# Optimization experiments

Measured on AMD Instinct MI355X. Metric: run time of the kernel, lower is better.

Reference implementation:

```python
import jax, jax.numpy as jnp
import numpy as np

N = 100000; NFEAT = 256; NHID = 128; NCLASS = 40; DEG = 16; E = N * DEG
L = 2; AH = 16; ALPHA = 0.2; LP_ALPHA = 0.5


def setup_inputs() -> dict:
    key = jax.random.key(0)
    ks = jax.random.split(key, 12)
    s = 0.05
    x = jax.random.normal(ks[0], (N, NFEAT), jnp.float32)
    row = jnp.repeat(jnp.arange(N), DEG)                       # each node has DEG out-edges
    col = jax.random.randint(ks[1], (E,), 0, N)
    edges = jnp.stack([row, col])                              # [2, E]
    degree = jax.random.uniform(ks[2], (N, 1), jnp.float32, 0.5, 1.5)
    label = jax.random.uniform(ks[3], (N, NCLASS), jnp.float32)
    return {
        "x": x, "edges": edges, "degree": degree, "iftrain": 0, "label": label,
        "lb_w": jax.random.normal(ks[4], (NHID, NFEAT)) * s,
        "lb_b": jnp.zeros((NHID,)),
        "L2F": jax.random.normal(ks[5], (NCLASS, NHID)) * s,
        "Ws": jax.random.normal(ks[6], (L, 2 * NHID, NHID)) * s,
        "w2m": jax.random.normal(ks[7], (L, AH, NHID)) * s,
        "b2m": jnp.zeros((L, AH)),
        "ab": jnp.zeros((L, 1, AH + 1)),
        "lf1w": jax.random.normal(ks[8], (L, AH, (AH + 1) * 3)) * s,
        "lf1b": jnp.zeros((L, AH)),
        "lf2w": jax.random.normal(ks[9], (L, 1, AH)) * s,
        "lf2b": jnp.zeros((L, 1)),
        "LPW": jnp.ones((L, N, 1)),
        "la2w": jax.random.normal(ks[10], (NCLASS, NHID)) * s,
        "la2b": jnp.zeros((NCLASS,)),
    }


def _seg(vals, row, n):
    return jax.ops.segment_sum(vals, row, num_segments=n)


def _layer(x, pre_label, aggr, row, col, degree, lpw, W, w2m, b2m, ab, lf1w, lf1b, lf2w, lf2b):
    n = x.shape[0]
    # final_h = aggr * spmm(adj, LP_W*h*deg) * deg + (1-aggr) * h
    h = jnp.concatenate([x, pre_label], axis=1) @ W            # [N, nhid]
    agg = _seg((lpw * h * degree)[col], row, n)
    h = aggr * agg * degree + (1.0 - aggr) * h
    rowcnt = _seg(jnp.ones((row.shape[0], 1), x.dtype), row, n)  # [N,1] edges per row

    def mini(feat):
        m = feat @ w2m.T + b2m                                 # [N, AH]
        avg = _seg(m[col], row, n) / rowcnt                    # mean neighbor feature
        dist = jnp.sqrt(jnp.sum((avg[row] - m[col]) ** 2, -1) + 1e-12)  # [E]
        d2 = (_seg(dist, row, n) / rowcnt[:, 0])[:, None]      # row-wise mean distance
        return jnp.concatenate([m, d2], axis=1)                # [N, AH+1]

    def factor(hs, hd, hdiff):
        f = jnp.tanh(jnp.concatenate([hs, hd, hdiff], 1) @ lf1w.T + lf1b)
        return jax.nn.sigmoid((f @ lf2w.T + lf2b)[:, 0])       # [E]

    m0 = mini(h)
    hs0, hd0 = m0[row], m0[col]
    hdiff = jnp.abs(hd0 - hs0)
    f0 = factor(hs0, hd0, hdiff)
    m1 = mini(x)
    f1 = factor(m1[row] + ab, m1[col] + ab, hdiff)             # note: reuses hdiff (as in torch code)
    f1hop = (_seg(f1, row, n) / rowcnt[:, 0])[:, None]         # mean-reduce spmm
    f2hop = (_seg(f0 * f1hop[col, 0], row, n) / rowcnt[:, 0])[:, None]
    return jax.nn.leaky_relu(h, ALPHA), f2hop


def reference(x, edges, degree, iftrain, label, lb_w, lb_b, L2F, Ws, w2m, b2m, ab,
              lf1w, lf1b, lf2w, lf2b, LPW, la2w, la2b):
    row, col = edges[0], edges[1]
    h = x @ lb_w.T + lb_b
    pre_label = label @ L2F
    aggr = jnp.asarray(LP_ALPHA, h.dtype)
    for l in range(L):
        h, aggr = _layer(h, pre_label, aggr, row, col, degree, LPW[l], Ws[l],
                         w2m[l], b2m[l], ab[l], lf1w[l], lf1b[l], lf2w[l], lf2b[l])
    return jax.nn.log_softmax(h @ la2w.T + la2b, axis=-1)
```

## Files before the change

kernel.cpp:

```cpp
#include <hip/hip_runtime.h>
#include <hip/hip_bf16.h>
#include <hip/hip_fp8.h>
#include <math.h>

#define NN 100000
#define NCLS 40
#define DEGC 16
#define NEDGE (NN*DEGC)
#define ALPHAC 0.2f
#define LPALPHA 0.5f

typedef short short8v __attribute__((ext_vector_type(8)));
typedef float f32x4 __attribute__((ext_vector_type(4)));

__device__ __forceinline__ short f2bf(float f) {
    unsigned u = __float_as_uint(f);
    u += 0x7fff + ((u >> 16) & 1);
    return (short)(u >> 16);
}
__device__ __forceinline__ float bf2f(ushort u) {
    return __uint_as_float(((unsigned)u) << 16);
}
__device__ __forceinline__ unsigned char f2e4m3(float f) {
    __hip_fp8_e4m3 e(f);
    return (unsigned char)e.__x;
}
__device__ __forceinline__ void e4m3x4(unsigned u, float* o) {
#pragma unroll
    for (int s = 0; s < 4; ++s) {
        __hip_fp8_e4m3 e;
        e.__x = (__hip_fp8_storage_t)((u >> (8 * s)) & 0xff);
        o[s] = (float)e;
    }
}

template <int NCH1, bool ABF, bool HASL, bool WRT8>
__global__ __launch_bounds__(256) void gemm128_lds(
    const void* __restrict__ A1v, const ushort* __restrict__ B1t,
    const ushort* __restrict__ labB64, const ushort* __restrict__ B2t,
    const float* __restrict__ bias, int leakyA, ushort* __restrict__ C,
    unsigned char* __restrict__ T8)
{
    constexpr int K1 = NCH1 * 32;
    constexpr int NG = NCH1 / 4;
    constexpr int NCH = NCH1 + (HASL ? 2 : 0);
    __shared__ __align__(16) ushort Bs1[128 * 128];
    __shared__ __align__(16) ushort Bs2[HASL ? 128 * 64 : 8];

    const int tid = threadIdx.x;
    const int l   = tid & 63;
    const int w   = tid >> 6;
    const int lr  = l & 15;
    const int lk8 = (l >> 4) << 3;
    const int n0  = blockIdx.x * 64 + w * 16;
    int r = n0 + lr; r = r < NN ? r : NN - 1;
    const int swz = (lr & 7) << 4;

    short8v afr[NCH];
    if (ABF) {
        const ushort* __restrict__ A = (const ushort*)A1v;
#pragma unroll
        for (int kc = 0; kc < NCH1; ++kc)
            afr[kc] = *(const short8v*)(A + (size_t)r * K1 + kc * 32 + lk8);
    } else {
        const float* __restrict__ A = (const float*)A1v;
#pragma unroll
        for (int g = 0; g < NCH1; g += 2) {
            const float* p0 = A + (size_t)r * K1 + g * 32 + lk8;
            const float* p1 = A + (size_t)r * K1 + (g + 1) * 32 + lk8;
            float4 a0 = *(const float4*)p0;
            float4 a1 = *(const float4*)(p0 + 4);
            float4 b0 = *(const float4*)p1;
            float4 b1 = *(const float4*)(p1 + 4);
            short8v va, vb;
            va[0] = f2bf(a0.x); va[1] = f2bf(a0.y); va[2] = f2bf(a0.z); va[3] = f2bf(a0.w);
            va[4] = f2bf(a1.x); va[5] = f2bf(a1.y); va[6] = f2bf(a1.z); va[7] = f2bf(a1.w);
            vb[0] = f2bf(b0.x); vb[1] = f2bf(b0.y); vb[2] = f2bf(b0.z); vb[3] = f2bf(b0.w);
            vb[4] = f2bf(b1.x); vb[5] = f2bf(b1.y); vb[6] = f2bf(b1.z); vb[7] = f2bf(b1.w);
            afr[g] = va;
            afr[g + 1] = vb;
        }
    }
    if (HASL) {
        afr[NCH1]     = *(const short8v*)(labB64 + (size_t)r * 64 + lk8);
        afr[NCH1 + 1] = *(const short8v*)(labB64 + (size_t)r * 64 + 32 + lk8);
    }
    if (ABF && leakyA) {
#pragma unroll
        for (int kc = 0; kc < NCH1; ++kc)
#pragma unroll
            for (int j = 0; j < 8; ++j) {
                float f = bf2f((ushort)afr[kc][j]);
                f = f > 0.f ? f : ALPHAC * f;
                afr[kc][j] = f2bf(f);
            }
    }

    if (HASL) {
#pragma unroll
        for (int s = 0; s < 4; ++s) {
            const int slot = tid + s * 256;
            const int row = slot >> 3, colq = slot & 7;
            uint4 v = *(const uint4*)(B2t + (size_t)row * 64 + colq * 8);
            *(uint4*)((char*)Bs2 + ((row * 128 + colq * 16) ^ ((row & 7) << 4))) = v;
        }
    }

    f32x4 acc[8];
#pragma unroll
    for (int ni = 0; ni < 8; ++ni) acc[ni] = (f32x4){0.f, 0.f, 0.f, 0.f};

#pragma unroll
    for (int g = 0; g < NG; ++g) {
        if (g) __syncthreads();
#pragma unroll
        for (int s = 0; s < 8; ++s) {
            const int slot = tid + s * 256;
            const int row = slot >> 4, colq = slot & 15;
            uint4 v = *(const uint4*)(B1t + (size_t)row * K1 + g * 128 + colq * 8);
            *(uint4*)((char*)Bs1 + ((row * 256 + colq * 16) ^ ((row & 7) << 4))) = v;
        }
        __syncthreads();
#pragma unroll
        for (int ni = 0; ni < 8; ++ni) {
#pragma unroll
            for (int kc = 0; kc < 4; ++kc) {
                short8v b = *(const short8v*)((const char*)Bs1 +
                    (((ni * 16 + lr) * 256 + kc * 64 + lk8 * 2) ^ swz));
                acc[ni] = __builtin_amdgcn_mfma_f32_16x16x32_bf16(afr[g * 4 + kc], b, acc[ni], 0, 0, 0);
            }
        }
    }
    if (HASL) {
#pragma unroll
        for (int ni = 0; ni < 8; ++ni) {
#pragma unroll
            for (int kc = 0; kc < 2; ++kc) {
                short8v b = *(const short8v*)((const char*)Bs2 +
                    (((ni * 16 + lr) * 128 + kc * 64 + lk8 * 2) ^ swz));
                acc[ni] = __builtin_amdgcn_mfma_f32_16x16x32_bf16(afr[NCH1 + kc], b, acc[ni], 0, 0, 0);
            }
        }
    }

    const int rsub = (l >> 4) << 2;
#pragma unroll
    for (int ni = 0; ni < 8; ++ni) {
        const int cc = ni * 16 + lr;
        const float bv = bias ? bias[cc] : 0.f;
#pragma unroll
        for (int rg = 0; rg < 4; ++rg) {
            const int rr = n0 + rsub + rg;
            if (rr < NN) {
                const float v = acc[ni][rg] + bv;
                C[(size_t)rr * 128 + cc] = (ushort)f2bf(v);
                if (WRT8) T8[(size_t)rr * 128 + cc] = f2e4m3(v);
            }
        }
    }
}

__global__ __launch_bounds__(256) void agg_v5(
    const unsigned char* __restrict__ T8, const ushort* __restrict__ hlin,
    const int* __restrict__ col, const float* __restrict__ sd,
    const float* __restrict__ degree, const float* __restrict__ aggrv,
    const float aggrs, int do_leaky, ushort* __restrict__ hout)
{
    const int lane = threadIdx.x & 63;
    const int node = blockIdx.x * 4 + (threadIdx.x >> 6);
    const int q  = lane >> 4;
    const int cq = lane & 15;

    int cl = 0; float sl = 0.f;
    if (lane < 16) {
        cl = col[node * 16 + lane];
        sl = sd[cl];
    }

    float ax[8];
#pragma unroll
    for (int s = 0; s < 8; ++s) ax[s] = 0.f;

#pragma unroll
    for (int g = 0; g < 4; ++g) {
        const int nb = g * 4 + q;
        const int   c  = __shfl(cl, nb, 64);
        const float wv = __shfl(sl, nb, 64);
        const uint2 u = *(const uint2*)(T8 + (size_t)c * 128 + cq * 8);
        float d0[4], d1[4];
        e4m3x4(u.x, d0);
        e4m3x4(u.y, d1);
#pragma unroll
        for (int s2 = 0; s2 < 4; ++s2) {
            ax[s2]     += wv * d0[s2];
            ax[4 + s2] += wv * d1[s2];
        }
    }
#pragma unroll
    for (int s = 0; s < 8; ++s) {
        ax[s] += __shfl_xor(ax[s], 16, 64);
        ax[s] += __shfl_xor(ax[s], 32, 64);
    }

    const uint4 us = *(const uint4*)(hlin + (size_t)node * 128 + cq * 8);
    const unsigned uus[4] = {us.x, us.y, us.z, us.w};
    const float a = aggrv ? aggrv[node] : aggrs;
    const float d = degree[node];
    uint4 uo;
    unsigned* uop = &uo.x;
#pragma unroll
    for (int s = 0; s < 4; ++s) {
        const int sx = (s >> 1) * 4 + (s & 1) * 2;
        float ox = a * ax[(s < 2 ? s * 2 : (s - 2) * 2 + 4)] * d;
        float oy = a * ax[(s < 2 ? s * 2 + 1 : (s - 2) * 2 + 5)] * d;
        ox += (1.f - a) * bf2f((ushort)(uus[s] & 0xffff));
        oy += (1.f - a) * bf2f((ushort)(uus[s] >> 16));
        if (do_leaky) {
            ox = ox > 0.f ? ox : ALPHAC * ox;
            oy = oy > 0.f ? oy : ALPHAC * oy;
        }
        uop[s] = (unsigned)(ushort)f2bf(ox) | ((unsigned)(ushort)f2bf(oy) << 16);
    }
    if (q == 0)
        *(uint4*)(hout + (size_t)node * 128 + cq * 8) = uo;
}

__global__ __launch_bounds__(256) void gemm16_mfma(
    const ushort* __restrict__ A, const ushort* __restrict__ Wb,
    const float* __restrict__ bias, ushort* __restrict__ Mout, int ooff)
{
    __shared__ __align__(16) ushort Wl[16 * 128];
    const int tid = threadIdx.x;
    const int l  = tid & 63;
    const int w  = tid >> 6;
    const int lr = l & 15;
    const int lk = (l >> 4) << 3;
    const int swz = (lr & 7) << 4;
    {
        const int row = tid >> 4, colq = tid & 15;
        uint4 v = *(const uint4*)(Wb + (size_t)row * 128 + colq * 8);
        *(uint4*)((char*)Wl + ((row * 256 + colq * 16) ^ ((row & 7) << 4))) = v;
    }
    const int n0 = blockIdx.x * 64 + w * 16;
    int ar = n0 + lr; ar = ar < NN ? ar : NN - 1;
    short8v a[4];
#pragma unroll
    for (int kc = 0; kc < 4; ++kc)
        a[kc] = *(const short8v*)(A + (size_t)ar * 128 + kc * 32 + lk);
    __syncthreads();
    f32x4 acc = (f32x4){0.f, 0.f, 0.f, 0.f};
#pragma unroll
    for (int kc = 0; kc < 4; ++kc) {
        short8v b = *(const short8v*)((const char*)Wl + ((lr * 256 + kc * 64 + lk * 2) ^ swz));
        acc = __builtin_amdgcn_mfma_f32_16x16x32_bf16(a[kc], b, acc, 0, 0, 0);
    }
    const float bv = bias[lr];
    const int rb = n0 + ((l >> 4) << 2);
#pragma unroll
    for (int r = 0; r < 4; ++r) {
        int rr = rb + r;
        if (rr < NN) Mout[(size_t)rr * 32 + ooff + lr] = (ushort)f2bf(acc[r] + bv);
    }
}

__global__ __launch_bounds__(256) void mini2_dual(
    const ushort* __restrict__ Mb01, const int* __restrict__ col,
    float* __restrict__ d2_0, float* __restrict__ d2_1)
{
    __shared__ float sm0[16][16][17];
    __shared__ float sm1[16][16][17];
    __shared__ float av0[16][16];
    __shared__ float av1[16][16];
    const int tid = threadIdx.x;
    const int g = tid >> 4, j = tid & 15;
    const int node = blockIdx.x * 16 + g;
    const int c = col[node * 16 + j];
    const ushort* __restrict__ rowp = Mb01 + (size_t)c * 32;
    const uint4 u0 = *(const uint4*)rowp;
    const uint4 u1 = *(const uint4*)(rowp + 8);
    const uint4 u2 = *(const uint4*)(rowp + 16);
    const uint4 u3 = *(const uint4*)(rowp + 24);
    const unsigned w0[8] = {u0.x, u0.y, u0.z, u0.w, u1.x, u1.y, u1.z, u1.w};
    const unsigned w1[8] = {u2.x, u2.y, u2.z, u2.w, u3.x, u3.y, u3.z, u3.w};
#pragma unroll
    for (int s = 0; s < 8; ++s) {
        sm0[g][j][s * 2]     = bf2f((ushort)(w0[s] & 0xffff));
        sm0[g][j][s * 2 + 1] = bf2f((ushort)(w0[s] >> 16));
        sm1[g][j][s * 2]     = bf2f((ushort)(w1[s] & 0xffff));
        sm1[g][j][s * 2 + 1] = bf2f((ushort)(w1[s] >> 16));
    }
    __syncthreads();
    float a0 = 0.f, a1 = 0.f;
#pragma unroll
    for (int nb = 0; nb < 16; ++nb) { a0 += sm0[g][nb][j]; a1 += sm1[g][nb][j]; }
    av0[g][j] = a0 * (1.f / 16.f);
    av1[g][j] = a1 * (1.f / 16.f);
    __syncthreads();
    float dd0 = 1e-12f, dd1 = 1e-12f;
#pragma unroll
    for (int d = 0; d < 16; ++d) {
        float t0 = av0[g][d] - sm0[g][j][d];
        float t1 = av1[g][d] - sm1[g][j][d];
        dd0 += t0 * t0;
        dd1 += t1 * t1;
    }
    float dist0 = sqrtf(dd0), dist1 = sqrtf(dd1);
#pragma unroll
    for (int off = 1; off < 16; off <<= 1) {
        dist0 += __shfl_xor(dist0, off, 64);
        dist1 += __shfl_xor(dist1, off, 64);
    }
    if (j == 0) {
        d2_0[node] = dist0 * (1.f / 16.f);
        d2_1[node] = dist1 * (1.f / 16.f);
    }
}

__global__ __launch_bounds__(256) void prep_pnode(
    const ushort* __restrict__ Mb01, const float* __restrict__ d2_0,
    const float* __restrict__ d2_1,
    const float* __restrict__ ab, const float* __restrict__ lf1w,
    const float* __restrict__ lf1b,
    float* __restrict__ P0s, float* __restrict__ P1s,
    unsigned char* __restrict__ PK8)
{
    const int idx = blockIdx.x * 256 + threadIdx.x;
    const int i = idx >> 4, k = idx & 15;
    float m0[17], m1a[17];
    const ushort* r0 = Mb01 + (size_t)i * 32;
    const ushort* r1 = r0 + 16;
#pragma unroll
    for (int d = 0; d < 16; ++d) {
        m0[d]  = bf2f(r0[d]);
        m1a[d] = bf2f(r1[d]) + ab[d];
    }
    m0[16]  = d2_0[i];
    m1a[16] = d2_1[i] + ab[16];
    const float* __restrict__ Wk = lf1w + k * 51;
    float p0s = lf1b[k], p1s = p0s, p0d = 0.f, p1d = 0.f;
#pragma unroll
    for (int d = 0; d < 17; ++d) {
        const float w0 = Wk[d], w1 = Wk[17 + d];
        p0s += m0[d]  * w0;  p0d += m0[d]  * w1;
        p1s += m1a[d] * w0;  p1d += m1a[d] * w1;
    }
    P0s[idx] = p0s;
    P1s[idx] = p1s;
    unsigned char* __restrict__ pk = PK8 + (size_t)i * 64;
    pk[k]      = f2e4m3(m0[k]);
    pk[16 + k] = f2e4m3(p0d);
    pk[32 + k] = f2e4m3(p1d);
    if (k == 0) *(float*)(pk + 48) = d2_0[i];
}

__global__ __launch_bounds__(256) void fact2_kernel(
    const unsigned char* __restrict__ PK8,
    const float* __restrict__ P0s, const float* __restrict__ P1s,
    const int* __restrict__ col,
    const float* __restrict__ W2c, const float* __restrict__ lf2w,
    const float* __restrict__ lf2b,
    float* __restrict__ f0out, float* __restrict__ f1hout)
{
    const int e = blockIdx.x * 256 + threadIdx.x;
    const int i = e >> 4;
    const int c = col[e];

    const unsigned char* __restrict__ pki = PK8 + (size_t)i * 64;
    const unsigned char* __restrict__ pkc = PK8 + (size_t)c * 64;
    const uint4 mi8 = *(const uint4*)pki;
    const float d2i = *(const float*)(pki + 48);
    const uint4 mc8 = *(const uint4*)pkc;
    const uint4 p08 = *(const uint4*)(pkc + 16);
    const uint4 p18 = *(const uint4*)(pkc + 32);
    const float d2c = *(const float*)(pkc + 48);

    float mi[16], mc[16], P0d[16], P1d[16];
    e4m3x4(mi8.x, mi);     e4m3x4(mi8.y, mi + 4);
    e4m3x4(mi8.z, mi + 8); e4m3x4(mi8.w, mi + 12);
    e4m3x4(mc8.x, mc);     e4m3x4(mc8.y, mc + 4);
    e4m3x4(mc8.z, mc + 8); e4m3x4(mc8.w, mc + 12);
    e4m3x4(p08.x, P0d);     e4m3x4(p08.y, P0d + 4);
    e4m3x4(p08.z, P0d + 8); e4m3x4(p08.w, P0d + 12);
    e4m3x4(p18.x, P1d);     e4m3x4(p18.y, P1d + 4);
    e4m3x4(p18.z, P1d + 8); e4m3x4(p18.w, P1d + 12);

    float2 H2[8];
#pragma unroll
    for (int k2 = 0; k2 < 8; ++k2) H2[k2] = make_float2(0.f, 0.f);
#pragma unroll
    for (int d = 0; d < 16; ++d) {
        const float hd = fabsf(mc[d] - mi[d]);
        const float2* __restrict__ wv = (const float2*)(W2c + d * 16);
#pragma unroll
        for (int k2 = 0; k2 < 8; ++k2) {
            H2[k2].x = fmaf(hd, wv[k2].x, H2[k2].x);
            H2[k2].y = fmaf(hd, wv[k2].y, H2[k2].y);
        }
    }
    {
        const float hdd = fabsf(d2c - d2i);
        const float2* __restrict__ wv = (const float2*)(W2c + 16 * 16);
#pragma unroll
        for (int k2 = 0; k2 < 8; ++k2) {
            H2[k2].x = fmaf(hdd, wv[k2].x, H2[k2].x);
            H2[k2].y = fmaf(hdd, wv[k2].y, H2[k2].y);
        }
    }
    const float* __restrict__ H = (const float*)H2;

    const float* __restrict__ p0 = P0s + (size_t)i * 16;
    const float* __restrict__ p1 = P1s + (size_t)i * 16;
    float a0 = lf2b[0], a1 = a0;
#pragma unroll
    for (int k = 0; k < 16; ++k) {
        const float t0 = p0[k] + P0d[k] + H[k];
        const float t1 = p1[k] + P1d[k] + H[k];
        const float lw = lf2w[k];
        a0 += (1.f - 2.f / (__expf(2.f * t0) + 1.f)) * lw;
        a1 += (1.f - 2.f / (__expf(2.f * t1) + 1.f)) * lw;
    }
    f0out[e] = 1.f / (1.f + __expf(-a0));
    float f1 = 1.f / (1.f + __expf(-a1));
#pragma unroll
    for (int off = 1; off < 16; off <<= 1) f1 += __shfl_xor(f1, off, 64);
    if ((threadIdx.x & 15) == 0) f1hout[i] = f1 * (1.f / 16.f);
}

__global__ void f2hop_kernel(const float* __restrict__ f0, const float* __restrict__ f1h,
                             const int* __restrict__ col, float* __restrict__ out)
{
    const int i = blockIdx.x * 256 + threadIdx.x;
    if (i >= NN) return;
    float s = 0.f;
#pragma unroll
    for (int t = 0; t < 16; ++t) {
        int e = i * 16 + t;
        s += f0[e] * f1h[col[e]];
    }
    out[i] = s * (1.f / 16.f);
}

__global__ __launch_bounds__(256) void logits_mfma(
    const ushort* __restrict__ X, const ushort* __restrict__ Wb48,
    const float* __restrict__ bias, float* __restrict__ out)
{
    __shared__ __align__(16) ushort Wl[48 * 128];
    const int tid = threadIdx.x;
    const int l  = tid & 63;
    const int w  = tid >> 6;
    const int lr = l & 15;
    const int lk = (l >> 4) << 3;
    const int swz = (lr & 7) << 4;
#pragma unroll
    for (int s = 0; s < 6; ++s) {
        const int slot = tid + s * 256;
        const int row = slot >> 4, colq = slot & 15;
        uint4 v = *(const uint4*)(Wb48 + (size_t)row * 128 + colq * 8);
        *(uint4*)((char*)Wl + ((row * 256 + colq * 16) ^ ((row & 7) << 4))) = v;
    }
    const int row_base = blockIdx.x * 128 + w * 32;
    short8v afr[2][4];
#pragma unroll
    for (int mi = 0; mi < 2; ++mi) {
        int r = row_base + mi * 16 + lr;
        r = r < NN ? r : NN - 1;
#pragma unroll
        for (int kc = 0; kc < 4; ++kc)
            afr[mi][kc] = *(const short8v*)(X + (size_t)r * 128 + kc * 32 + lk);
    }
    __syncthreads();
    f32x4 acc[2][3];
#pragma unroll
    for (int mi = 0; mi < 2; ++mi)
#pragma unroll
        for (int ni = 0; ni < 3; ++ni) acc[mi][ni] = (f32x4){0.f, 0.f, 0.f, 0.f};
#pragma unroll
    for (int ni = 0; ni < 3; ++ni) {
#pragma unroll
        for (int kc = 0; kc < 4; ++kc) {
            short8v b = *(const short8v*)((const char*)Wl +
                (((ni * 16 + lr) * 256 + kc * 64 + lk * 2) ^ swz));
#pragma unroll
            for (int mi = 0; mi < 2; ++mi)
                acc[mi][ni] = __builtin_amdgcn_mfma_f32_16x16x32_bf16(afr[mi][kc], b, acc[mi][ni], 0, 0, 0);
        }
    }

    const float b0 = bias[lr];
    const float b1 = bias[16 + lr];
    const float b2 = (lr < 8) ? bias[32 + lr] : 0.f;
    const int rsub = (l >> 4) << 2;
#pragma unroll
    for (int mi = 0; mi < 2; ++mi) {
#pragma unroll
        for (int reg = 0; reg < 4; ++reg) {
            const int row = row_base + mi * 16 + rsub + reg;
            const float z0 = acc[mi][0][reg] + b0;
            const float z1 = acc[mi][1][reg] + b1;
            const float z2 = (lr < 8) ? acc[mi][2][reg] + b2 : -1e30f;
            float m = fmaxf(fmaxf(z0, z1), z2);
#pragma unroll
            for (int off = 1; off < 16; off <<= 1) m = fmaxf(m, __shfl_xor(m, off, 64));
            float s = __expf(z0 - m) + __expf(z1 - m) + ((lr < 8) ? __expf(z2 - m) : 0.f);
#pragma unroll
            for (int off = 1; off < 16; off <<= 1) s += __shfl_xor(s, off, 64);
            const float lg = m + __logf(s);
            if (row < NN) {
                float* __restrict__ po = out + (size_t)row * NCLS;
                po[lr] = z0 - lg;
                po[16 + lr] = z1 - lg;
                if (lr < 8) po[32 + lr] = z2 - lg;
            }
        }
    }
}

__global__ void prep_misc(
    const float* __restrict__ lb_w, ushort* __restrict__ Bt0,
    const float* __restrict__ Ws, ushort* __restrict__ Wt1,
    const float* __restrict__ L2F, ushort* __restrict__ W2t,
    const float* __restrict__ la2w, ushort* __restrict__ Wb48,
    const float* __restrict__ lf1w, float* __restrict__ W2c,
    const float* __restrict__ w2m, ushort* __restrict__ W2mB,
    const float* __restrict__ LPW, const float* __restrict__ degree,
    float* __restrict__ sd2)
{
    int b = blockIdx.x;
    const int tid = threadIdx.x;
    if (b < 128) {
        int i = b * 256 + tid;
        Bt0[i] = (ushort)f2bf(lb_w[i]);
        return;
    }
    b -= 128;
    if (b < 128) {
        int i = b * 256 + tid;
        int ll = i >> 14, r = i & 16383;
        int m = r >> 7, k = r & 127;
        Wt1[i] = (ushort)f2bf(Ws[(size_t)ll * 32768 + k * 128 + m]);
        return;
    }
    b -= 128;
    if (b < 64) {
        int i = b * 256 + tid;
        int ll = i >> 13, r = i & 8191;
        int m = r >> 6, c = r & 63;
        float acc = 0.f;
        if (c < NCLS) {
            const float* Wl = Ws + (size_t)ll * 32768 + 128 * 128;
            for (int j = 0; j < 128; ++j) acc += L2F[c * 128 + j] * Wl[j * 128 + m];
        }
        W2t[i] = (ushort)f2bf(acc);
        return;
    }
    b -= 64;
    if (b < 24) {
        int i = b * 256 + tid;
        if (i < 48 * 128) {
            int c = i >> 7;
            Wb48[i] = (c < NCLS) ? (ushort)f2bf(la2w[i]) : (ushort)0;
        }
        return;
    }
    b -= 24;
    if (b < 2) {
        int t = b * 256 + tid;
        if (t < 272) {
            int d = t >> 4, k = t & 15;
            W2c[t] = lf1w[k * 51 + 34 + d];
        }
        return;
    }
    b -= 2;
    if (b < 8) {
        int i = b * 256 + tid;
        W2mB[i] = (ushort)f2bf(w2m[i]);
        return;
    }
    b -= 8;
    if (b < 391) {
        int i = b * 256 + tid;
        if (i < NN) sd2[i] = LPW[i] * degree[i];
        return;
    }
    b -= 391;
    {
        int i = b * 256 + tid;
        if (i < NN) sd2[NN + i] = LPW[NN + i] * degree[i];
    }
}

__global__ void cvt_label64v(const float* __restrict__ label, ushort* __restrict__ labB64)
{
    const int idx = blockIdx.x * 256 + threadIdx.x;
    const int i = idx >> 4;
    const int c0 = (idx & 15) * 4;
    ushort o[4];
#pragma unroll
    for (int j = 0; j < 4; ++j) {
        const int c = c0 + j;
        o[j] = (c < NCLS) ? (ushort)f2bf(label[(size_t)i * NCLS + c]) : (ushort)0;
    }
    *(uint2*)(labB64 + (size_t)i * 64 + c0) = make_uint2(
        (unsigned)o[0] | ((unsigned)o[1] << 16),
        (unsigned)o[2] | ((unsigned)o[3] << 16));
}

extern "C" void kernel_launch(void* const* d_in, const int* in_sizes, int n_in,
                              void* d_out, int out_size, void* d_ws, size_t ws_size,
                              hipStream_t stream)
{
    const float* x      = (const float*)d_in[0];
    const int*   edges  = (const int*)d_in[1];
    const float* degree = (const float*)d_in[2];
    const float* label  = (const float*)d_in[4];
    const float* lb_w   = (const float*)d_in[5];
    const float* lb_b   = (const float*)d_in[6];
    const float* L2F    = (const float*)d_in[7];
    const float* Ws     = (const float*)d_in[8];
    const float* w2m    = (const float*)d_in[9];
    const float* b2m    = (const float*)d_in[10];
    const float* ab     = (const float*)d_in[11];
    const float* lf1w   = (const float*)d_in[12];
    const float* lf1b   = (const float*)d_in[13];
    const float* lf2w   = (const float*)d_in[14];
    const float* lf2b   = (const float*)d_in[15];
    const float* LPW    = (const float*)d_in[16];
    const float* la2w   = (const float*)d_in[17];
    const float* la2b   = (const float*)d_in[18];
    const int* colp = edges + NEDGE;

    float* ws = (float*)d_ws;
    size_t o = 0;
    float* d2_0B = ws + o; o += NN;
    float* d2_1B = ws + o; o += NN;
    float* P0sB  = ws + o; o += (size_t)NN * 16;
    float* P1sB  = ws + o; o += (size_t)NN * 16;
    float* f0B   = ws + o; o += NEDGE;
    float* f1hB  = ws + o; o += NN;
    float* aggrB = ws + o; o += NN;
    float* sd2B  = ws + o; o += 2 * NN;
    float* W2cB  = ws + o; o += 272;
    ushort* bufA = (ushort*)(ws + o); o += (size_t)NN * 128 / 2;
    ushort* bufL = (ushort*)(ws + o); o += (size_t)NN * 128 / 2;
    ushort* labB64 = (ushort*)(ws + o); o += (size_t)NN * 64 / 2;
    ushort* Mb01 = (ushort*)(ws + o); o += (size_t)NN * 32 / 2;
    unsigned char* PK8 = (unsigned char*)(ws + o); o += (size_t)NN * 64 / 4;
    ushort* Bt0  = (ushort*)(ws + o); o += 128 * 256 / 2;
    ushort* Wt1  = (ushort*)(ws + o); o += 2 * 128 * 128 / 2;
    ushort* W2t  = (ushort*)(ws + o); o += 2 * 128 * 64 / 2;
    ushort* W2mB = (ushort*)(ws + o); o += 16 * 128 / 2;
    ushort* Wb48 = (ushort*)(ws + o); o += 48 * 128 / 2;
    unsigned char* T8 = (unsigned char*)(ws + o); o += (size_t)NN * 128 / 4;

    dim3 b256(256);
    prep_misc<<<1136, b256, 0, stream>>>(lb_w, Bt0, Ws, Wt1, L2F, W2t, la2w, Wb48,
                                         lf1w, W2cB, w2m, W2mB, LPW, degree, sd2B);
    cvt_label64v<<<6250, b256, 0, stream>>>(label, labB64);

    gemm128_lds<8, false, false, false><<<1563, b256, 0, stream>>>(
        x, Bt0, nullptr, nullptr, lb_b, 0, bufA, nullptr);

    gemm128_lds<4, true, true, true><<<1563, b256, 0, stream>>>(
        bufA, Wt1, labB64, W2t, nullptr, 0, bufL, T8);
    gemm16_mfma<<<1563, b256, 0, stream>>>(bufA, W2mB, b2m, Mb01, 16);
    agg_v5<<<25000, b256, 0, stream>>>(T8, bufL, colp, sd2B, degree,
                                       nullptr, LPALPHA, 0, bufA);
    gemm16_mfma<<<1563, b256, 0, stream>>>(bufA, W2mB, b2m, Mb01, 0);
    mini2_dual<<<6250, b256, 0, stream>>>(Mb01, colp, d2_0B, d2_1B);
    prep_pnode<<<6250, b256, 0, stream>>>(Mb01, d2_0B, d2_1B, ab, lf1w, lf1b,
                                          P0sB, P1sB, PK8);
    fact2_kernel<<<6250, b256, 0, stream>>>(PK8, P0sB, P1sB, colp,
                                            W2cB, lf2w, lf2b, f0B, f1hB);
    f2hop_kernel<<<391, b256, 0, stream>>>(f0B, f1hB, colp, aggrB);

    gemm128_lds<4, true, true, true><<<1563, b256, 0, stream>>>(
        bufA, Wt1 + 16384, labB64, W2t + 8192, nullptr, 1, bufL, T8);
    agg_v5<<<25000, b256, 0, stream>>>(T8, bufL, colp, sd2B + NN, degree,
                                       aggrB, 0.f, 1, bufA);

    logits_mfma<<<782, b256, 0, stream>>>(bufA, Wb48, la2b, (float*)d_out);
}
```

Before: 357.6 us.

## Fold input linear layer into layer-0 GEMM and mini projection via precomposed weights

Precomputes the products of lb_w with the layer-0 W and with w2m, plus the matching biases, in the prep kernel. Layer 0's GEMM and the m1 projection then run directly on x with K=256. This removes the separate lb GEMM, its write and re-read of a 100000x128 intermediate, and one gemm16 launch. The cost is extra LDS rows and MFMAs in the fused kernel, plus a slow scalar weight composition in prep. It also changes rounding, because the intermediate h is no longer rounded to bf16.

```diff
diff --git a/kernel.cpp b/kernel.cpp
--- a/kernel.cpp
+++ b/kernel.cpp
@@ -34,17 +34,20 @@
     }
 }
 
-template <int NCH1, bool ABF, bool HASL, bool WRT8>
+template <int NCH1, bool ABF, bool HASL, bool WRT8, bool HASM1>
 __global__ __launch_bounds__(256) void gemm128_lds(
     const void* __restrict__ A1v, const ushort* __restrict__ B1t,
     const ushort* __restrict__ labB64, const ushort* __restrict__ B2t,
-    const float* __restrict__ bias, int leakyA, ushort* __restrict__ C,
-    unsigned char* __restrict__ T8)
+    const float* __restrict__ bias, const float* __restrict__ biasm1,
+    int leakyA, ushort* __restrict__ C,
+    unsigned char* __restrict__ T8, ushort* __restrict__ M1out)
 {
     constexpr int K1 = NCH1 * 32;
     constexpr int NG = NCH1 / 4;
     constexpr int NCH = NCH1 + (HASL ? 2 : 0);
-    __shared__ __align__(16) ushort Bs1[128 * 128];
+    constexpr int BROWS = HASM1 ? 144 : 128;
+    constexpr int NSLOT = BROWS / 16;
+    __shared__ __align__(16) ushort Bs1[BROWS * 128];
     __shared__ __align__(16) ushort Bs2[HASL ? 128 * 64 : 8];
 
     const int tid = threadIdx.x;
@@ -109,12 +112,13 @@
     f32x4 acc[8];
 #pragma unroll
     for (int ni = 0; ni < 8; ++ni) acc[ni] = (f32x4){0.f, 0.f, 0.f, 0.f};
+    f32x4 accm1 = (f32x4){0.f, 0.f, 0.f, 0.f};
 
 #pragma unroll
     for (int g = 0; g < NG; ++g) {
         if (g) __syncthreads();
 #pragma unroll
-        for (int s = 0; s < 8; ++s) {
+        for (int s = 0; s < NSLOT; ++s) {
             const int slot = tid + s * 256;
             const int row = slot >> 4, colq = slot & 15;
             uint4 v = *(const uint4*)(B1t + (size_t)row * K1 + g * 128 + colq * 8);
@@ -128,6 +132,14 @@
                 short8v b = *(const short8v*)((const char*)Bs1 +
                     (((ni * 16 + lr) * 256 + kc * 64 + lk8 * 2) ^ swz));
                 acc[ni] = __builtin_amdgcn_mfma_f32_16x16x32_bf16(afr[g * 4 + kc], b, acc[ni], 0, 0, 0);
+            }
+        }
+        if (HASM1) {
+#pragma unroll
+            for (int kc = 0; kc < 4; ++kc) {
+                short8v b = *(const short8v*)((const char*)Bs1 +
+                    (((128 + lr) * 256 + kc * 64 + lk8 * 2) ^ swz));
+                accm1 = __builtin_amdgcn_mfma_f32_16x16x32_bf16(afr[g * 4 + kc], b, accm1, 0, 0, 0);
             }
         }
     }
@@ -156,6 +168,15 @@
                 C[(size_t)rr * 128 + cc] = (ushort)f2bf(v);
                 if (WRT8) T8[(size_t)rr * 128 + cc] = f2e4m3(v);
             }
+        }
+    }
+    if (HASM1) {
+        const float bm = biasm1[lr];
+#pragma unroll
+        for (int rg = 0; rg < 4; ++rg) {
+            const int rr = n0 + rsub + rg;
+            if (rr < NN)
+                M1out[(size_t)rr * 32 + 16 + lr] = (ushort)f2bf(accm1[rg] + bm);
         }
     }
 }
@@ -210,7 +231,6 @@
     unsigned* uop = &uo.x;
 #pragma unroll
     for (int s = 0; s < 4; ++s) {
-        const int sx = (s >> 1) * 4 + (s & 1) * 2;
         float ox = a * ax[(s < 2 ? s * 2 : (s - 2) * 2 + 4)] * d;
         float oy = a * ax[(s < 2 ? s * 2 + 1 : (s - 2) * 2 + 5)] * d;
         ox += (1.f - a) * bf2f((ushort)(uus[s] & 0xffff));
@@ -516,23 +536,19 @@
 }
 
 __global__ void prep_misc(
-    const float* __restrict__ lb_w, ushort* __restrict__ Bt0,
+    const float* __restrict__ lb_w, const float* __restrict__ lb_b,
     const float* __restrict__ Ws, ushort* __restrict__ Wt1,
     const float* __restrict__ L2F, ushort* __restrict__ W2t,
     const float* __restrict__ la2w, ushort* __restrict__ Wb48,
     const float* __restrict__ lf1w, float* __restrict__ W2c,
     const float* __restrict__ w2m, ushort* __restrict__ W2mB,
+    const float* __restrict__ b2m,
     const float* __restrict__ LPW, const float* __restrict__ degree,
-    float* __restrict__ sd2)
+    float* __restrict__ sd2, ushort* __restrict__ B1x,
+    float* __restrict__ bias1, float* __restrict__ bm1e)
 {
     int b = blockIdx.x;
     const int tid = threadIdx.x;
-    if (b < 128) {
-        int i = b * 256 + tid;
-        Bt0[i] = (ushort)f2bf(lb_w[i]);
-        return;
-    }
-    b -= 128;
     if (b < 128) {
         int i = b * 256 + tid;
         int ll = i >> 14, r = i & 16383;
@@ -584,9 +600,43 @@
         return;
     }
     b -= 391;
-    {
+    if (b < 391) {
         int i = b * 256 + tid;
         if (i < NN) sd2[NN + i] = LPW[NN + i] * degree[i];
+        return;
+    }
+    b -= 391;
+    if (b < 128) {
+        int i = b * 256 + tid;
+        int m = i >> 8, k = i & 255;
+        float acc = 0.f;
+        for (int mp = 0; mp < 128; ++mp)
+            acc += lb_w[mp * 256 + k] * Ws[mp * 128 + m];
+        B1x[(size_t)m * 256 + k] = (ushort)f2bf(acc);
+        return;
+    }
+    b -= 128;
+    if (b < 16) {
+        int i = b * 256 + tid;
+        int j = i >> 8, k = i & 255;
+        float acc = 0.f;
+        for (int mp = 0; mp < 128; ++mp)
+            acc += lb_w[mp * 256 + k] * w2m[j * 128 + mp];
+        B1x[(size_t)(128 + j) * 256 + k] = (ushort)f2bf(acc);
+        return;
+    }
+    b -= 16;
+    {
+        if (tid < 128) {
+            float acc = 0.f;
+            for (int mp = 0; mp < 128; ++mp) acc += lb_b[mp] * Ws[mp * 128 + tid];
+            bias1[tid] = acc;
+        } else if (tid < 144) {
+            const int j = tid - 128;
+            float acc = b2m[j];
+            for (int mp = 0; mp < 128; ++mp) acc += lb_b[mp] * w2m[j * 128 + mp];
+            bm1e[j] = acc;
+        }
     }
 }
 
@@ -641,12 +691,14 @@
     float* aggrB = ws + o; o += NN;
     float* sd2B  = ws + o; o += 2 * NN;
     float* W2cB  = ws + o; o += 272;
+    float* bias1B = ws + o; o += 128;
+    float* bm1eB  = ws + o; o += 16;
     ushort* bufA = (ushort*)(ws + o); o += (size_t)NN * 128 / 2;
     ushort* bufL = (ushort*)(ws + o); o += (size_t)NN * 128 / 2;
     ushort* labB64 = (ushort*)(ws + o); o += (size_t)NN * 64 / 2;
     ushort* Mb01 = (ushort*)(ws + o); o += (size_t)NN * 32 / 2;
     unsigned char* PK8 = (unsigned char*)(ws + o); o += (size_t)NN * 64 / 4;
-    ushort* Bt0  = (ushort*)(ws + o); o += 128 * 256 / 2;
+    ushort* B1x  = (ushort*)(ws + o); o += 144 * 256 / 2;
     ushort* Wt1  = (ushort*)(ws + o); o += 2 * 128 * 128 / 2;
     ushort* W2t  = (ushort*)(ws + o); o += 2 * 128 * 64 / 2;
     ushort* W2mB = (ushort*)(ws + o); o += 16 * 128 / 2;
@@ -654,16 +706,13 @@
     unsigned char* T8 = (unsigned char*)(ws + o); o += (size_t)NN * 128 / 4;
 
     dim3 b256(256);
-    prep_misc<<<1136, b256, 0, stream>>>(lb_w, Bt0, Ws, Wt1, L2F, W2t, la2w, Wb48,
-                                         lf1w, W2cB, w2m, W2mB, LPW, degree, sd2B);
+    prep_misc<<<1153, b256, 0, stream>>>(lb_w, lb_b, Ws, Wt1, L2F, W2t, la2w, Wb48,
+                                         lf1w, W2cB, w2m, W2mB, b2m, LPW, degree,
+                                         sd2B, B1x, bias1B, bm1eB);
     cvt_label64v<<<6250, b256, 0, stream>>>(label, labB64);
 
-    gemm128_lds<8, false, false, false><<<1563, b256, 0, stream>>>(
-        x, Bt0, nullptr, nullptr, lb_b, 0, bufA, nullptr);
-
-    gemm128_lds<4, true, true, true><<<1563, b256, 0, stream>>>(
-        bufA, Wt1, labB64, W2t, nullptr, 0, bufL, T8);
-    gemm16_mfma<<<1563, b256, 0, stream>>>(bufA, W2mB, b2m, Mb01, 16);
+    gemm128_lds<8, false, true, true, true><<<1563, b256, 0, stream>>>(
+        x, B1x, labB64, W2t, bias1B, bm1eB, 0, bufL, T8, Mb01);
     agg_v5<<<25000, b256, 0, stream>>>(T8, bufL, colp, sd2B, degree,
                                        nullptr, LPALPHA, 0, bufA);
     gemm16_mfma<<<1563, b256, 0, stream>>>(bufA, W2mB, b2m, Mb01, 0);
@@ -674,8 +723,8 @@
                                             W2cB, lf2w, lf2b, f0B, f1hB);
     f2hop_kernel<<<391, b256, 0, stream>>>(f0B, f1hB, colp, aggrB);
 
-    gemm128_lds<4, true, true, true><<<1563, b256, 0, stream>>>(
-        bufA, Wt1 + 16384, labB64, W2t + 8192, nullptr, 1, bufL, T8);
+    gemm128_lds<4, true, true, true, false><<<1563, b256, 0, stream>>>(
+        bufA, Wt1 + 16384, labB64, W2t + 8192, nullptr, nullptr, 1, bufL, T8, nullptr);
     agg_v5<<<25000, b256, 0, stream>>>(T8, bufL, colp, sd2B + NN, degree,
                                        aggrB, 0.f, 1, bufA);
 
```

Measured after the change: 310.5 us. -13.2%, faster.
